# Kernel optimization log

Hardware: AMD Instinct MI355X
Metric: run time of the kernel (lower is better)

## Reference

```python
import jax, jax.numpy as jnp
import numpy as np

N = 262144
IF = 256   # indiv_f_dim
CF = 256   # collab_f_dim
D = IF + CF  # d_model = 512
EMB = 256
NUM_SEASONS = 8192


def setup_inputs() -> dict:
    key = jax.random.key(0)
    ks = jax.random.split(key, 20)
    inp = {
        'indiv_f': jax.random.normal(ks[0], (N, IF), jnp.float32),
        'hierarchy_f': jax.random.normal(ks[1], (N, CF), jnp.float32),
        'strength_f': jax.random.normal(ks[2], (N, CF), jnp.float32),
        'recency_f': jax.random.normal(ks[3], (N, CF), jnp.float32),
        'season_ids': jax.random.randint(ks[4], (N,), 0, NUM_SEASONS, jnp.int32),
    }
    s = 0.02
    # Attention_Biased_Walk: attn_fc1 (no bias)
    inp['w_attn1'] = jax.random.normal(ks[5], (1, 2 * CF), jnp.float32) * s
    # MultiHeadAttention (heads=1): q,k,v,out linears (torch Linear: [out,in] + bias)
    inp['Wq'] = jax.random.normal(ks[6], (D, D), jnp.float32) * s
    inp['bq'] = jnp.zeros((D,), jnp.float32)
    inp['Wk'] = jax.random.normal(ks[7], (D, D), jnp.float32) * s
    inp['bk'] = jnp.zeros((D,), jnp.float32)
    inp['Wv'] = jax.random.normal(ks[8], (D, D), jnp.float32) * s
    inp['bv'] = jnp.zeros((D,), jnp.float32)
    inp['Wo'] = jax.random.normal(ks[9], (D, D), jnp.float32) * s
    inp['bo'] = jnp.zeros((D,), jnp.float32)
    # fc: d_model -> emb_dim
    inp['Wfc'] = jax.random.normal(ks[10], (EMB, D), jnp.float32) * s
    inp['bfc'] = jnp.zeros((EMB,), jnp.float32)
    # output_fc: emb_dim -> 1
    inp['Wout'] = jax.random.normal(ks[11], (1, EMB), jnp.float32) * s
    inp['bout'] = jnp.zeros((1,), jnp.float32)
    return inp


def _forward(indiv_f, hierarchy_f, strength_f, recency_f,
             w_attn1, Wq, bq, Wk, bk, Wv, bv, Wo, bo,
             Wfc, bfc, Wout, bout, season_ids):
    H, S, R = hierarchy_f, strength_f, recency_f
    # Attention_Biased_Walk (is_hierarchy & is_strength & is_recency all True).
    # Dropout is identity in eval. leaky_relu default slope 0.01.
    def e(a, b):
        return jax.nn.leaky_relu(jnp.concatenate([a, b], axis=1) @ w_attn1.T, 0.01)  # [N,1]
    e_all = jnp.stack([e(H, S), e(H, R), e(H, H)], axis=2)          # [N,1,3]
    alpha = jax.nn.softmax(e_all, axis=2)                            # [N,1,3]
    v_cand = jnp.stack([S, R, H], axis=2)                            # [N,CF,3]
    agg_collab_f = jnp.sum(alpha * v_cand, axis=2)                   # [N,CF]

    x = jnp.concatenate([indiv_f, agg_collab_f], axis=1)            # [N,D]

    # MultiHeadAttention with bs=n_members, seq_len=1 per member:
    # scores is [bs,1,1,1], softmax over size-1 axis == 1, so attn = v-projection.
    q = x @ Wq.T + bq
    k = x @ Wk.T + bk
    v = x @ Wv.T + bv
    d_k = D  # heads = 1
    scores = jnp.sum(q * k, axis=-1, keepdims=True) / jnp.sqrt(jnp.float32(d_k))  # [N,1]
    attn_w = jax.nn.softmax(scores[..., None], axis=-1)[..., 0]     # == 1.0, kept for fidelity
    attn_out = (attn_w * v) @ Wo.T + bo                              # [N,D]

    member_emb = jax.nn.relu(attn_out @ Wfc.T + bfc)                 # [N,EMB]

    # Per-season mean-pool (vectorized equivalent of the python loop; all seasons present).
    sums = jax.ops.segment_sum(member_emb, season_ids, num_segments=NUM_SEASONS)
    counts = jax.ops.segment_sum(jnp.ones((member_emb.shape[0],), member_emb.dtype),
                                 season_ids, num_segments=NUM_SEASONS)
    team_emb = sums / jnp.maximum(counts, 1.0)[:, None]              # [NUM_SEASONS,EMB]

    return team_emb @ Wout.T + bout                                  # [NUM_SEASONS,1]


def reference(indiv_f, hierarchy_f, strength_f, recency_f, season_ids,
              w_attn1, Wq, bq, Wk, bk, Wv, bv, Wo, bo, Wfc, bfc, Wout, bout):
    return _forward(indiv_f, hierarchy_f, strength_f, recency_f,
                    w_attn1, Wq, bq, Wk, bk, Wv, bv, Wo, bo,
                    Wfc, bfc, Wout, bout, season_ids)
```

## Files before the change

kernel.cpp:

```cpp
#include <hip/hip_runtime.h>
#include <hip/hip_bf16.h>

typedef __bf16 v8bf __attribute__((ext_vector_type(8)));
typedef __bf16 v4bf __attribute__((ext_vector_type(4)));
typedef float  v4f  __attribute__((ext_vector_type(4)));

#define NMEM 262144
#define CFD  256
#define NSEA 8192



__global__ void gemm_nn(const float* __restrict__ A, const float* __restrict__ B,
                        float* __restrict__ C, int M, int Nn, int K) {
  __shared__ float As[16][17];
  __shared__ float Bs[16][17];
  const int tx = threadIdx.x, ty = threadIdx.y;
  const int row = blockIdx.y * 16 + ty;
  const int col = blockIdx.x * 16 + tx;
  float acc = 0.f;
  for (int kk = 0; kk < K; kk += 16) {
    As[ty][tx] = A[row * K + kk + tx];
    Bs[ty][tx] = B[(kk + ty) * Nn + col];
    __syncthreads();
#pragma unroll
    for (int t = 0; t < 16; ++t) acc += As[ty][t] * Bs[t][tx];
    __syncthreads();
  }
  C[row * Nn + col] = acc;
}

__global__ void bias_dot(const float* __restrict__ W, const float* __restrict__ x,
                         const float* __restrict__ b, float* __restrict__ o, int K) {
  const int i = blockIdx.x, L = threadIdx.x;
  const float* row = W + (size_t)i * K;
  float s = 0.f;
  for (int k = L; k < K; k += 64) s += row[k] * x[k];
#pragma unroll
  for (int m = 32; m; m >>= 1) s += __shfl_xor(s, m, 64);
  if (L == 0) o[i] = s + b[i];
}

__global__ void pack_b(const float* __restrict__ W3, __bf16* __restrict__ Bp) {
  const int t = blockIdx.x * 256 + threadIdx.x;
  const int L = t & 63, kc = (t >> 6) & 15, nt = t >> 10;
  const int n = nt * 16 + (L & 15);
  const int k = kc * 32 + ((L >> 4) << 3);
  const float* src = W3 + n * 512 + k;
  __bf16* dst = Bp + (size_t)t * 8;
#pragma unroll
  for (int j = 0; j < 8; ++j) dst[j] = (__bf16)src[j];
}


__global__ __launch_bounds__(256, 2)
void fused_main(const float* __restrict__ indiv,
                const float* __restrict__ hier,
                const float* __restrict__ stren,
                const float* __restrict__ rec,
                const int*   __restrict__ sid,
                const float* __restrict__ w1,
                const __bf16* __restrict__ Bp,
                const float* __restrict__ b3,
                const float* __restrict__ wout,
                float* __restrict__ sums,
                float* __restrict__ counts) {
  __shared__ __bf16 xhi[4][16][264];
  __shared__ v8bf  btile[16 * 64];

  const int tid = threadIdx.x;
  const int w = tid >> 6, L = tid & 63;
  const int mbase = blockIdx.x * 64 + w * 16;

  const float4 w1a = *(const float4*)(w1 + 4 * L);
  const float4 w1b = *(const float4*)(w1 + 256 + 4 * L);

  const float* hrow = hier  + (size_t)mbase * CFD + 4 * L;
  const float* srow = stren + (size_t)mbase * CFD + 4 * L;
  const float* rrow = rec   + (size_t)mbase * CFD + 4 * L;
  float4 Hc = *(const float4*)hrow;
  float4 Sc = *(const float4*)srow;
  float4 Rc = *(const float4*)rrow;
  for (int i = 0; i < 16; ++i) {
    const int nx = (i < 15) ? (i + 1) : 15;
    float4 Hn = *(const float4*)(hrow + nx * CFD);
    float4 Sn = *(const float4*)(srow + nx * CFD);
    float4 Rn = *(const float4*)(rrow + nx * CFD);

    const float pHa = w1a.x*Hc.x + w1a.y*Hc.y + w1a.z*Hc.z + w1a.w*Hc.w;
    const float pSb = w1b.x*Sc.x + w1b.y*Sc.y + w1b.z*Sc.z + w1b.w*Sc.w;
    const float pRb = w1b.x*Rc.x + w1b.y*Rc.y + w1b.z*Rc.z + w1b.w*Rc.w;
    const float pHb = w1b.x*Hc.x + w1b.y*Hc.y + w1b.z*Hc.z + w1b.w*Hc.w;
    float q1 = pHa + pSb;
    float q2 = pHa + pRb;
    float q3 = pHa + pHb;
#pragma unroll
    for (int m = 32; m; m >>= 1) {
      q1 += __shfl_xor(q1, m, 64);
      q2 += __shfl_xor(q2, m, 64);
      q3 += __shfl_xor(q3, m, 64);
    }
    const float e1 = q1 > 0.f ? q1 : 0.01f * q1;
    const float e2 = q2 > 0.f ? q2 : 0.01f * q2;
    const float e3 = q3 > 0.f ? q3 : 0.01f * q3;
    const float mx = fmaxf(e1, fmaxf(e2, e3));
    float a1 = __expf(e1 - mx), a2 = __expf(e2 - mx), a3 = __expf(e3 - mx);
    const float inv = 1.f / (a1 + a2 + a3);
    a1 *= inv; a2 *= inv; a3 *= inv;

    v4bf g;
    g[0] = (__bf16)(a1 * Sc.x + a2 * Rc.x + a3 * Hc.x);
    g[1] = (__bf16)(a1 * Sc.y + a2 * Rc.y + a3 * Hc.y);
    g[2] = (__bf16)(a1 * Sc.z + a2 * Rc.z + a3 * Hc.z);
    g[3] = (__bf16)(a1 * Sc.w + a2 * Rc.w + a3 * Hc.w);
    *(v4bf*)&xhi[w][i][4 * L] = g;

    Hc = Hn; Sc = Sn; Rc = Rn;
  }

  const int ml = L & 15;
  const int qo = (L >> 4) * 8;
  v8bf af[16];
  {
    const float* ip = indiv + (size_t)(mbase + ml) * CFD;
#pragma unroll
    for (int c = 0; c < 8; ++c) {
      const float4 f0 = *(const float4*)(ip + c * 32 + qo);
      const float4 f1 = *(const float4*)(ip + c * 32 + qo + 4);
      v8bf t;
      t[0] = (__bf16)f0.x; t[1] = (__bf16)f0.y; t[2] = (__bf16)f0.z; t[3] = (__bf16)f0.w;
      t[4] = (__bf16)f1.x; t[5] = (__bf16)f1.y; t[6] = (__bf16)f1.z; t[7] = (__bf16)f1.w;
      af[c] = t;
    }
#pragma unroll
    for (int c = 0; c < 8; ++c)
      af[8 + c] = *(const v8bf*)&xhi[w][ml][c * 32 + qo];
  }

  float p0 = 0.f, p1 = 0.f, p2 = 0.f, p3 = 0.f;
  const uint4* bsrc = (const uint4*)Bp;
  uint4* bl = (uint4*)btile;
  for (int nt = 0; nt < 16; ++nt) {
    __syncthreads();
#pragma unroll
    for (int j = 0; j < 4; ++j)
      bl[tid + j * 256] = bsrc[nt * 1024 + tid + j * 256];
    __syncthreads();

    v4f acc = {0.f, 0.f, 0.f, 0.f};
#pragma unroll
    for (int c = 0; c < 16; ++c) {
      const v8bf bf = btile[c * 64 + L];
      acc = __builtin_amdgcn_mfma_f32_16x16x32_bf16(af[c], bf, acc, 0, 0, 0);
    }
    const float b3n = b3[nt * 16 + ml];
    const float wn  = wout[nt * 16 + ml];
    p0 += fmaxf(acc[0] + b3n, 0.f) * wn;
    p1 += fmaxf(acc[1] + b3n, 0.f) * wn;
    p2 += fmaxf(acc[2] + b3n, 0.f) * wn;
    p3 += fmaxf(acc[3] + b3n, 0.f) * wn;
  }

#pragma unroll
  for (int m = 8; m; m >>= 1) {
    p0 += __shfl_xor(p0, m, 64);
    p1 += __shfl_xor(p1, m, 64);
    p2 += __shfl_xor(p2, m, 64);
    p3 += __shfl_xor(p3, m, 64);
  }
  const int r = ml;
  if (r < 4) {
    const float pv = (r == 0) ? p0 : (r == 1) ? p1 : (r == 2) ? p2 : p3;
    const int mem = mbase + (L >> 4) * 4 + r;
    const int s = sid[mem];
    atomicAdd(&sums[s], pv);
    atomicAdd(&counts[s], 1.0f);
  }
}

__global__ void finalize_k(const float* __restrict__ sums,
                           const float* __restrict__ counts,
                           const float* __restrict__ bout,
                           float* __restrict__ out) {
  const int s = blockIdx.x * 256 + threadIdx.x;
  if (s < NSEA) out[s] = sums[s] / fmaxf(counts[s], 1.0f) + bout[0];
}


extern "C" void kernel_launch(void* const* d_in, const int* in_sizes, int n_in,
                              void* d_out, int out_size, void* d_ws, size_t ws_size,
                              hipStream_t stream) {
  (void)in_sizes; (void)n_in; (void)out_size; (void)ws_size;
  const float* indiv = (const float*)d_in[0];
  const float* hier  = (const float*)d_in[1];
  const float* stren = (const float*)d_in[2];
  const float* rec   = (const float*)d_in[3];
  const int*   sid   = (const int*)d_in[4];
  const float* w1    = (const float*)d_in[5];
  const float* Wv    = (const float*)d_in[10];
  const float* bv    = (const float*)d_in[11];
  const float* Wo    = (const float*)d_in[12];
  const float* bo    = (const float*)d_in[13];
  const float* Wfc   = (const float*)d_in[14];
  const float* bfc   = (const float*)d_in[15];
  const float* wout  = (const float*)d_in[16];
  const float* bout  = (const float*)d_in[17];
  float* out = (float*)d_out;

  char* ws = (char*)d_ws;
  float*  T1   = (float*)(ws + 0);
  float*  W3   = (float*)(ws + 1048576);
  float*  bc   = (float*)(ws + 1572864);
  float*  b3   = (float*)(ws + 1574912);
  __bf16* Bp   = (__bf16*)(ws + 1575936);
  float*  sums = (float*)(ws + 1838080);
  float*  cnts = (float*)(ws + 1870848);

  hipMemsetAsync(ws + 1838080, 0, 65536, stream);

  dim3 b16(16, 16);
  gemm_nn<<<dim3(32, 32), b16, 0, stream>>>(Wo,  Wv, T1, 512, 512, 512);
  bias_dot<<<512, 64, 0, stream>>>(Wo, bv, bo, bc, 512);
  gemm_nn<<<dim3(32, 16), b16, 0, stream>>>(Wfc, T1, W3, 256, 512, 512);
  bias_dot<<<256, 64, 0, stream>>>(Wfc, bc, bfc, b3, 512);
  pack_b<<<64, 256, 0, stream>>>(W3, Bp);

  fused_main<<<NMEM / 64, 256, 0, stream>>>(indiv, hier, stren, rec, sid, w1,
                                            Bp, b3, wout, sums, cnts);
  finalize_k<<<NSEA / 256, 256, 0, stream>>>(sums, cnts, bout, out);
}
```

Before: 936.2 us.

## Alias fused kernel LDS buffers with swizzle and register-tile the weight-folding GEMM

The fused kernel's separate xhi and btile shared arrays are merged into one 32 KB aliased buffer. The B tile reuses the region after the gathered activations have been loaded into registers, and the activation writes and reads use an XOR-swizzled layout to avoid LDS bank conflicts. Launch bounds rise from 2 to 5 blocks per SM so more waves can hide the memory-bound streaming loads, at the risk of register spills. The small precompute GEMM moves to 64x64 tiles with 4x4 register blocking per thread, which cuts its launch count and shared-memory traffic.

```diff
diff --git a/kernel.cpp b/kernel.cpp
--- a/kernel.cpp
+++ b/kernel.cpp
@@ -11,23 +11,44 @@
 
 
 
-__global__ void gemm_nn(const float* __restrict__ A, const float* __restrict__ B,
-                        float* __restrict__ C, int M, int Nn, int K) {
-  __shared__ float As[16][17];
-  __shared__ float Bs[16][17];
-  const int tx = threadIdx.x, ty = threadIdx.y;
-  const int row = blockIdx.y * 16 + ty;
-  const int col = blockIdx.x * 16 + tx;
-  float acc = 0.f;
+__global__ __launch_bounds__(256)
+void gemm_nn(const float* __restrict__ A, const float* __restrict__ B,
+             float* __restrict__ C, int M, int Nn, int K) {
+  __shared__ float As[16][68];
+  __shared__ float Bs[16][68];
+  const int tid = threadIdx.x;
+  const int tx = tid & 15, ty = tid >> 4;
+  const int row0 = blockIdx.y * 64, col0 = blockIdx.x * 64;
+  const int lr = tid >> 2, lk = (tid & 3) << 2;
+  const int br = tid >> 4, bc = (tid & 15) << 2;
+  float acc[4][4] = {};
   for (int kk = 0; kk < K; kk += 16) {
-    As[ty][tx] = A[row * K + kk + tx];
-    Bs[ty][tx] = B[(kk + ty) * Nn + col];
-    __syncthreads();
-#pragma unroll
-    for (int t = 0; t < 16; ++t) acc += As[ty][t] * Bs[t][tx];
-    __syncthreads();
-  }
-  C[row * Nn + col] = acc;
+    const float4 a4 = *(const float4*)(A + (size_t)(row0 + lr) * K + kk + lk);
+    const float4 b4 = *(const float4*)(B + (size_t)(kk + br) * Nn + col0 + bc);
+    __syncthreads();
+    As[lk + 0][lr] = a4.x; As[lk + 1][lr] = a4.y;
+    As[lk + 2][lr] = a4.z; As[lk + 3][lr] = a4.w;
+    *(float4*)&Bs[br][bc] = b4;
+    __syncthreads();
+#pragma unroll
+    for (int t = 0; t < 16; ++t) {
+      const float4 av = *(const float4*)&As[t][ty << 2];
+      const float4 bv = *(const float4*)&Bs[t][tx << 2];
+      acc[0][0] += av.x * bv.x; acc[0][1] += av.x * bv.y;
+      acc[0][2] += av.x * bv.z; acc[0][3] += av.x * bv.w;
+      acc[1][0] += av.y * bv.x; acc[1][1] += av.y * bv.y;
+      acc[1][2] += av.y * bv.z; acc[1][3] += av.y * bv.w;
+      acc[2][0] += av.z * bv.x; acc[2][1] += av.z * bv.y;
+      acc[2][2] += av.z * bv.z; acc[2][3] += av.z * bv.w;
+      acc[3][0] += av.w * bv.x; acc[3][1] += av.w * bv.y;
+      acc[3][2] += av.w * bv.z; acc[3][3] += av.w * bv.w;
+    }
+  }
+#pragma unroll
+  for (int i = 0; i < 4; ++i) {
+    const float4 o = make_float4(acc[i][0], acc[i][1], acc[i][2], acc[i][3]);
+    *(float4*)(C + (size_t)(row0 + (ty << 2) + i) * Nn + col0 + (tx << 2)) = o;
+  }
 }
 
 __global__ void bias_dot(const float* __restrict__ W, const float* __restrict__ x,
@@ -53,7 +74,7 @@
 }
 
 
-__global__ __launch_bounds__(256, 2)
+__global__ __launch_bounds__(256, 5)
 void fused_main(const float* __restrict__ indiv,
                 const float* __restrict__ hier,
                 const float* __restrict__ stren,
@@ -65,12 +86,12 @@
                 const float* __restrict__ wout,
                 float* __restrict__ sums,
                 float* __restrict__ counts) {
-  __shared__ __bf16 xhi[4][16][264];
-  __shared__ v8bf  btile[16 * 64];
+  __shared__ __align__(16) char smem[32768];
 
   const int tid = threadIdx.x;
   const int w = tid >> 6, L = tid & 63;
   const int mbase = blockIdx.x * 64 + w * 16;
+  __bf16* const xw = (__bf16*)(smem + (w << 13));
 
   const float4 w1a = *(const float4*)(w1 + 4 * L);
   const float4 w1b = *(const float4*)(w1 + 256 + 4 * L);
@@ -113,7 +134,11 @@
     g[1] = (__bf16)(a1 * Sc.y + a2 * Rc.y + a3 * Hc.y);
     g[2] = (__bf16)(a1 * Sc.z + a2 * Rc.z + a3 * Hc.z);
     g[3] = (__bf16)(a1 * Sc.w + a2 * Rc.w + a3 * Hc.w);
-    *(v4bf*)&xhi[w][i][4 * L] = g;
+    {
+      const int u  = ((L >> 3) << 6) | (((L >> 1) & 3) << 4) | i;
+      const int us = u ^ ((u >> 4) & 7);
+      *(v4bf*)(xw + us * 8 + ((L & 1) << 2)) = g;
+    }
 
     Hc = Hn; Sc = Sn; Rc = Rn;
   }
@@ -133,13 +158,17 @@
       af[c] = t;
     }
 #pragma unroll
-    for (int c = 0; c < 8; ++c)
-      af[8 + c] = *(const v8bf*)&xhi[w][ml][c * 32 + qo];
+    for (int c = 0; c < 8; ++c) {
+      const int u  = (c << 6) | L;
+      const int us = u ^ ((u >> 4) & 7);
+      af[8 + c] = *(const v8bf*)(xw + us * 8);
+    }
   }
 
   float p0 = 0.f, p1 = 0.f, p2 = 0.f, p3 = 0.f;
   const uint4* bsrc = (const uint4*)Bp;
-  uint4* bl = (uint4*)btile;
+  uint4* bl = (uint4*)smem;
+  const v8bf* btile = (const v8bf*)smem;
   for (int nt = 0; nt < 16; ++nt) {
     __syncthreads();
 #pragma unroll
@@ -218,10 +247,9 @@
 
   hipMemsetAsync(ws + 1838080, 0, 65536, stream);
 
-  dim3 b16(16, 16);
-  gemm_nn<<<dim3(32, 32), b16, 0, stream>>>(Wo,  Wv, T1, 512, 512, 512);
+  gemm_nn<<<dim3(8, 8), 256, 0, stream>>>(Wo,  Wv, T1, 512, 512, 512);
   bias_dot<<<512, 64, 0, stream>>>(Wo, bv, bo, bc, 512);
-  gemm_nn<<<dim3(32, 16), b16, 0, stream>>>(Wfc, T1, W3, 256, 512, 512);
+  gemm_nn<<<dim3(8, 4), 256, 0, stream>>>(Wfc, T1, W3, 256, 512, 512);
   bias_dot<<<256, 64, 0, stream>>>(Wfc, bc, bfc, b3, 512);
   pack_b<<<64, 256, 0, stream>>>(W3, Bp);
 
```

Measured after the change: 1.016 ms. +8.5%, slower.
